# Kernel tuning notes

Hardware: AMD Instinct MI355X
Metric: run time of the kernel (lower is better)

## Reference

```python
import jax, jax.numpy as jnp
import numpy as np

NUM_ENTITIES = 100000
NUM_RELATIONS = 500
D = 256            # embedding_dim
T = 4              # num_hash_tables
H = 32             # hash_dim
B = 64             # batch of queries
K = 10
CAND = max(K * 10, int(NUM_ENTITIES * 0.1))  # = 10000


def setup_inputs() -> dict:
    key = jax.random.key(0)
    k0, k1, k2, k3, k4 = jax.random.split(key, 5)
    return {
        "head": jax.random.randint(k0, (B,), 0, NUM_ENTITIES),
        "relation": jax.random.randint(k1, (B,), 0, NUM_RELATIONS),
        "entity_emb": jax.random.normal(k2, (NUM_ENTITIES, D), jnp.float32) * 0.02,
        "relation_emb": jax.random.normal(k3, (NUM_RELATIONS, D), jnp.float32) * 0.02,
        "hash_proj": jax.random.normal(k4, (T, D, H), jnp.float32),
        "k": K,
    }


def reference(head, relation, entity_emb, relation_emb, hash_proj, k):
    # DistMult approximate query path of KnowledgeGraph.query (use_approximate=True).
    h = entity_emb[head]            # [B, D]
    r = relation_emb[relation]      # [B, D]
    target = h * r                  # DistMult target embedding [B, D]

    # LSH hash codes (0/1 floats): projected > 0
    thash = (jnp.einsum('bd,tdh->bth', target, hash_proj) > 0).astype(jnp.float32)      # [B,T,H]
    ahash = (jnp.einsum('nd,tdh->nth', entity_emb, hash_proj) > 0).astype(jnp.float32)  # [N,T,H]

    # Hamming distance over (T,H) bits without materializing [B,N,T,H]:
    # mismatches = sum(a) + sum(b) - 2 * <a,b>  for 0/1 codes
    dot = jnp.einsum('bth,nth->bn', thash, ahash)                                        # [B,N]
    hash_dist = thash.sum((1, 2))[:, None] + ahash.sum((1, 2))[None, :] - 2.0 * dot      # [B,N]

    # top num_candidates with SMALLEST hamming distance
    _, cand_idx = jax.lax.top_k(-hash_dist, CAND)                                        # [B,CAND]

    # DistMult score: (h*r*t).sum(-1) == target . t ; compute dense then gather candidates
    scores_all = jnp.einsum('bd,nd->bn', target, entity_emb)                             # [B,N]
    cand_scores = jnp.take_along_axis(scores_all, cand_idx, axis=1)                      # [B,CAND]

    top_scores, top_local = jax.lax.top_k(cand_scores, k)                                # [B,k]
    top_indices = jnp.take_along_axis(cand_idx, top_local, axis=1)                       # [B,k]
    return top_indices, top_scores
```

## Files before the change

### kernel.cpp

```cpp
#include <hip/hip_runtime.h>
#include <hip/hip_bf16.h>
#include <float.h>

constexpr int NENT  = 100000;
constexpr int DDIM  = 256;
constexpr int BQ    = 64;
constexpr int CANDN = 10000;
constexpr int KTOP  = 10;
constexpr int NSLICE = 16;
constexpr int SLICE  = 6272;
constexpr int HPAD   = 132;

typedef short v8s __attribute__((ext_vector_type(8)));
typedef float v4f __attribute__((ext_vector_type(4)));

__device__ inline void split3(float x, unsigned short& h0, unsigned short& h1,
                              unsigned short& h2) {
    unsigned t0 = __float_as_uint(x) & 0xffff0000u;
    float r1 = x - __uint_as_float(t0);
    unsigned t1 = __float_as_uint(r1) & 0xffff0000u;
    float r2 = r1 - __uint_as_float(t1);
    h0 = (unsigned short)(t0 >> 16);
    h1 = (unsigned short)(t1 >> 16);
    h2 = (unsigned short)(__float_as_uint(r2) >> 16);
}

__device__ inline void split8(const float* ap, v8s& o0, v8s& o1, v8s& o2) {
    union { v8s v; unsigned short u[8]; } r0, r1, r2;
    float4 f0 = *(const float4*)ap;
    float4 f1 = *(const float4*)(ap + 4);
    float av[8] = {f0.x, f0.y, f0.z, f0.w, f1.x, f1.y, f1.z, f1.w};
    #pragma unroll
    for (int j = 0; j < 8; j++)
        split3(av[j], r0.u[j], r1.u[j], r2.u[j]);
    o0 = r0.v; o1 = r1.v; o2 = r2.v;
}

__global__ __launch_bounds__(128) void k_targets(
    const int* __restrict__ head, const int* __restrict__ rel,
    const float* __restrict__ E, const float* __restrict__ Rm,
    const float* __restrict__ proj,
    float* __restrict__ tgtT, unsigned* __restrict__ thash)
{
    __shared__ float tg[DDIM];
    int b = blockIdx.x;
    int tid = threadIdx.x;
    int h = head[b], r = rel[b];
    for (int d = tid; d < DDIM; d += 128) {
        float v = E[h*DDIM + d] * Rm[r*DDIM + d];
        tg[d] = v;
        tgtT[d*BQ + b] = v;
    }
    __syncthreads();
    int t = tid >> 5, hh = tid & 31;
    float acc = 0.f;
    #pragma unroll 8
    for (int d = 0; d < DDIM; d++)
        acc += tg[d] * proj[(t*DDIM + d)*32 + hh];
    unsigned long long m = __ballot(acc > 0.0f);
    int lane = tid & 63, w = tid >> 6;
    if (lane == 0) {
        thash[b*4 + w*2 + 0] = (unsigned)(m & 0xffffffffull);
        thash[b*4 + w*2 + 1] = (unsigned)(m >> 32);
    }
}

__global__ __launch_bounds__(256) void k_prepw(
    const float* __restrict__ proj, const float* __restrict__ tgtT,
    unsigned short* __restrict__ Whi, unsigned short* __restrict__ Wmid,
    unsigned short* __restrict__ Wlo)
{
    int c = blockIdx.x;
    int d = threadIdx.x;
    float x = (c < 128) ? proj[((c >> 5)*DDIM + d)*32 + (c & 31)]
                        : tgtT[d*BQ + (c - 128)];
    unsigned short h0, h1, h2;
    split3(x, h0, h1, h2);
    Whi [c*DDIM + d] = h0;
    Wmid[c*DDIM + d] = h1;
    Wlo [c*DDIM + d] = h2;
}

constexpr int TILE_E = 128;
constexpr int LSTR = 40;
constexpr int ASTR = 36;

__global__ __launch_bounds__(256, 2) void k_gemm(
    const float* __restrict__ E,
    const unsigned short* __restrict__ Whi, const unsigned short* __restrict__ Wmid,
    const unsigned short* __restrict__ Wlo,
    unsigned* __restrict__ ahash, float* __restrict__ scores)
{
    __shared__ __align__(16) float Af[TILE_E*ASTR];
    __shared__ __align__(16) unsigned short Bhi[192*LSTR];
    __shared__ __align__(16) unsigned short Bmid[192*LSTR];
    __shared__ __align__(16) unsigned short Blo[192*LSTR];
    unsigned short* bitsHalf = (unsigned short*)Af;

    int tid = threadIdx.x;
    int l = tid & 63, w = tid >> 6;
    int wm = w >> 1, wn = w & 1;
    int m = l & 15, quad = l >> 4;
    int n0 = blockIdx.x * TILE_E;

    v4f acc[4][6];
    #pragma unroll
    for (int a = 0; a < 4; a++)
        #pragma unroll
        for (int c = 0; c < 6; c++)
            acc[a][c] = (v4f)0.0f;

    for (int ch = 0; ch < DDIM/32; ch++) {
        int d0 = ch * 32;
        __syncthreads();
        #pragma unroll
        for (int it = 0; it < 4; it++) {
            int idx = tid + it*256;
            int row = idx >> 3;
            int kq  = (idx & 7) * 4;
            int n = n0 + row; if (n >= NENT) n = NENT - 1;
            *(float4*)&Af[row*ASTR + kq] = *(const float4*)(E + (size_t)n*DDIM + d0 + kq);
        }
        #pragma unroll
        for (int it = 0; it < 3; it++) {
            int idx = tid + it*256;
            int col = idx >> 2;
            int k8  = (idx & 3) * 8;
            *(uint4*)&Bhi [col*LSTR + k8] = *(const uint4*)(Whi  + col*DDIM + d0 + k8);
            *(uint4*)&Bmid[col*LSTR + k8] = *(const uint4*)(Wmid + col*DDIM + d0 + k8);
            *(uint4*)&Blo [col*LSTR + k8] = *(const uint4*)(Wlo  + col*DDIM + d0 + k8);
        }
        __syncthreads();
        v8s a0[4], a1[4], a2[4];
        #pragma unroll
        for (int a = 0; a < 4; a++)
            split8(&Af[(wm*64 + a*16 + m)*ASTR + quad*8], a0[a], a1[a], a2[a]);
        #pragma unroll
        for (int c = 0; c < 6; c++) {
            int co = (wn*96 + c*16 + m)*LSTR + quad*8;
            v8s b0 = *(const v8s*)&Bhi [co];
            v8s b1 = *(const v8s*)&Bmid[co];
            v8s b2 = *(const v8s*)&Blo [co];
            #pragma unroll
            for (int a = 0; a < 4; a++) {
                acc[a][c] = __builtin_amdgcn_mfma_f32_16x16x32_bf16(a2[a], b0, acc[a][c], 0, 0, 0);
                acc[a][c] = __builtin_amdgcn_mfma_f32_16x16x32_bf16(a0[a], b2, acc[a][c], 0, 0, 0);
                acc[a][c] = __builtin_amdgcn_mfma_f32_16x16x32_bf16(a1[a], b1, acc[a][c], 0, 0, 0);
                acc[a][c] = __builtin_amdgcn_mfma_f32_16x16x32_bf16(a1[a], b0, acc[a][c], 0, 0, 0);
                acc[a][c] = __builtin_amdgcn_mfma_f32_16x16x32_bf16(a0[a], b1, acc[a][c], 0, 0, 0);
                acc[a][c] = __builtin_amdgcn_mfma_f32_16x16x32_bf16(a0[a], b0, acc[a][c], 0, 0, 0);
            }
        }
    }

    __syncthreads();
    #pragma unroll
    for (int c = 0; c < 6; c++) {
        int ct = wn*6 + c;
        if (ct < 8) {
            #pragma unroll
            for (int a = 0; a < 4; a++) {
                #pragma unroll
                for (int r = 0; r < 4; r++) {
                    unsigned long long mb = __ballot(acc[a][c][r] > 0.0f);
                    if (m == 0) {
                        int rowl = wm*64 + a*16 + quad*4 + r;
                        bitsHalf[rowl*8 + ct] = (unsigned short)(mb >> (quad*16));
                    }
                }
            }
        } else {
            int b = ct*16 - 128 + m;
            #pragma unroll
            for (int a = 0; a < 4; a++) {
                int nb = n0 + wm*64 + a*16 + quad*4;
                if (nb < NENT)
                    *(float4*)(scores + (size_t)b*NENT + nb) = *(float4*)&acc[a][c];
            }
        }
    }
    __syncthreads();
    if (tid < TILE_E) {
        int n = n0 + tid;
        if (n < NENT)
            *(uint4*)(ahash + (size_t)n*4) = *(const uint4*)&bitsHalf[tid*8];
    }
}

__global__ __launch_bounds__(256) void k_dist(
    const unsigned* __restrict__ ahash, const unsigned* __restrict__ thash,
    unsigned char* __restrict__ dist8, unsigned short* __restrict__ histG)
{
    __shared__ unsigned hist[HPAD];
    int s = blockIdx.x, b = blockIdx.y, tid = threadIdx.x;
    for (int i = tid; i < HPAD; i += 256) hist[i] = 0u;
    uint4 tw = *(const uint4*)(thash + b*4);
    __syncthreads();
    int n0 = s*SLICE;
    int n1 = n0 + SLICE; if (n1 > NENT) n1 = NENT;
    unsigned char* drow = dist8 + (size_t)b*NENT;
    for (int n = n0 + tid*4; n < n1; n += 1024) {
        int dv[4];
        #pragma unroll
        for (int i = 0; i < 4; i++) {
            uint4 a = *(const uint4*)(ahash + (size_t)(n+i)*4);
            dv[i] = __popc(a.x^tw.x) + __popc(a.y^tw.y) +
                    __popc(a.z^tw.z) + __popc(a.w^tw.w);
            atomicAdd(&hist[dv[i]], 1u);
        }
        uchar4 o = make_uchar4((unsigned char)dv[0], (unsigned char)dv[1],
                               (unsigned char)dv[2], (unsigned char)dv[3]);
        *(uchar4*)(drow + n) = o;
    }
    __syncthreads();
    unsigned short* hrow = histG + ((size_t)b*NSLICE + s)*HPAD;
    for (int i = tid; i < 129; i += 256) hrow[i] = (unsigned short)hist[i];
}

__global__ __launch_bounds__(64) void k_cut(
    const unsigned char* __restrict__ dist8, const unsigned short* __restrict__ histG,
    int* __restrict__ dsG, int* __restrict__ ncG)
{
    __shared__ unsigned histT[HPAD];
    __shared__ int dsS, slS, rpS;
    int b = blockIdx.x, tid = threadIdx.x;
    for (int d = tid; d < 129; d += 64) {
        unsigned sum = 0;
        for (int s = 0; s < NSLICE; s++)
            sum += histG[((size_t)b*NSLICE + s)*HPAD + d];
        histT[d] = sum;
    }
    __syncthreads();
    if (tid == 0) {
        unsigned cum = 0; int ds = 128; unsigned R = 1;
        for (int d = 0; d < 129; d++) {
            unsigned c = cum + histT[d];
            if (c >= (unsigned)CANDN) { ds = d; R = (unsigned)CANDN - cum; break; }
            cum = c;
        }
        dsS = ds; dsG[b] = ds;
        unsigned acc = 0;
        for (int s = 0; s < NSLICE; s++) {
            unsigned c = histG[((size_t)b*NSLICE + s)*HPAD + ds];
            if (acc + c >= R) { slS = s; rpS = (int)(R - acc); break; }
            acc += c;
        }
    }
    __syncthreads();
    int ds = dsS;
    unsigned Rp = (unsigned)rpS;
    const unsigned char* drow = dist8 + (size_t)b*NENT;
    int sBase = slS*SLICE;
    int sEnd = sBase + SLICE; if (sEnd > NENT) sEnd = NENT;
    unsigned cnt = 0;
    for (int base = sBase; base < sEnd; base += 64) {
        int n = base + tid;
        bool eq = (n < sEnd) && (drow[n] == (unsigned char)ds);
        unsigned long long mm = __ballot(eq);
        unsigned c = __popcll(mm);
        if (cnt + c >= Rp) {
            unsigned pre = __popcll(mm & ((1ull << tid) - 1ull));
            if (eq && (cnt + pre + 1u == Rp)) ncG[b] = n;
            break;
        }
        cnt += c;
    }
}

__global__ __launch_bounds__(256) void k_part(
    const unsigned char* __restrict__ dist8, const float* __restrict__ scores,
    const int* __restrict__ dsG, const int* __restrict__ ncG,
    const float* __restrict__ tgtT, const float* __restrict__ E,
    float* __restrict__ partS, int* __restrict__ partI)
{
    __shared__ float rs[256];
    __shared__ int   ri[256];
    __shared__ int   rt[256];
    __shared__ int   chosenI[KTOP];
    __shared__ float tgl[DDIM];

    int sl = blockIdx.x, b = blockIdx.y, tid = threadIdx.x;
    int ds = dsG[b], nc = ncG[b];
    const unsigned char* drow = dist8 + (size_t)b*NENT;
    const float* srow = scores + (size_t)b*NENT;
    int n0 = sl*SLICE;
    int n1 = n0 + SLICE; if (n1 > NENT) n1 = NENT;

    float topS[KTOP]; int topI[KTOP];
    #pragma unroll
    for (int i = 0; i < KTOP; i++) { topS[i] = -FLT_MAX; topI[i] = 0x7fffffff; }

    for (int n = n0 + tid*4; n < n1; n += 1024) {
        uchar4 dv = *(const uchar4*)(drow + n);
        unsigned char da[4] = {dv.x, dv.y, dv.z, dv.w};
        #pragma unroll
        for (int i = 0; i < 4; i++) {
            int d = da[i];
            int nn = n + i;
            if (d < ds || (d == ds && nn <= nc)) {
                float sc = srow[nn];
                if (sc > topS[KTOP-1]) {
                    int p = KTOP - 1;
                    while (p > 0 && topS[p-1] < sc) {
                        topS[p] = topS[p-1]; topI[p] = topI[p-1]; p--;
                    }
                    topS[p] = sc; topI[p] = nn;
                }
            }
        }
    }

    int ph = 0;
    for (int r = 0; r < KTOP; r++) {
        rs[tid] = topS[ph]; ri[tid] = topI[ph]; rt[tid] = tid;
        __syncthreads();
        for (int st = 128; st > 0; st >>= 1) {
            if (tid < st) {
                bool take = (rs[tid+st] > rs[tid]) ||
                            (rs[tid+st] == rs[tid] && ri[tid+st] < ri[tid]);
                if (take) { rs[tid]=rs[tid+st]; ri[tid]=ri[tid+st]; rt[tid]=rt[tid+st]; }
            }
            __syncthreads();
        }
        if (tid == 0) {
            chosenI[r] = ri[0];
            partI[((size_t)b*NSLICE + sl)*KTOP + r] = ri[0];
        }
        int winner = rt[0];
        __syncthreads();
        if (tid == winner) ph++;
        __syncthreads();
    }

    for (int d = tid; d < DDIM; d += 256) tgl[d] = tgtT[d*BQ + b];
    __syncthreads();
    if (tid < KTOP) {
        int idx = chosenI[tid];
        float sc = -FLT_MAX;
        if (idx >= 0 && idx < NENT) {
            const float* er = E + (size_t)idx*DDIM;
            float acc = 0.f;
            #pragma unroll 8
            for (int d = 0; d < DDIM; d += 4) {
                float4 v = *(const float4*)(er + d);
                acc += v.x*tgl[d+0];
                acc += v.y*tgl[d+1];
                acc += v.z*tgl[d+2];
                acc += v.w*tgl[d+3];
            }
            sc = acc;
        }
        partS[((size_t)b*NSLICE + sl)*KTOP + tid] = sc;
    }
}

__global__ __launch_bounds__(256) void k_merge(
    const float* __restrict__ partS, const int* __restrict__ partI,
    float* __restrict__ out)
{
    __shared__ float sc2[NSLICE*KTOP];
    __shared__ int   ix2[NSLICE*KTOP];
    int b = blockIdx.x, tid = threadIdx.x;
    if (tid < NSLICE*KTOP) {
        sc2[tid] = partS[(size_t)b*NSLICE*KTOP + tid];
        ix2[tid] = partI[(size_t)b*NSLICE*KTOP + tid];
    }
    __syncthreads();
    if (tid < NSLICE*KTOP) {
        float mv = sc2[tid]; int mi = ix2[tid];
        int rank = 0;
        #pragma unroll 8
        for (int i = 0; i < NSLICE*KTOP; i++) {
            float v = sc2[i]; int id = ix2[i];
            bool beats = (v > mv) ||
                         (v == mv && (id < mi || (id == mi && i < tid)));
            rank += beats ? 1 : 0;
        }
        if (rank < KTOP) {
            out[b*KTOP + rank]           = (float)mi;
            out[BQ*KTOP + b*KTOP + rank] = mv;
        }
    }
}

extern "C" void kernel_launch(void* const* d_in, const int* in_sizes, int n_in,
                              void* d_out, int out_size, void* d_ws, size_t ws_size,
                              hipStream_t stream)
{
    const int*   head = (const int*)d_in[0];
    const int*   rel  = (const int*)d_in[1];
    const float* E    = (const float*)d_in[2];
    const float* Rm   = (const float*)d_in[3];
    const float* proj = (const float*)d_in[4];

    char* ws = (char*)d_ws;
    float*          tgtT   = (float*)(ws);
    unsigned*       thash  = (unsigned*)(ws + 65536);
    unsigned*       ahash  = (unsigned*)(ws + 66560);
    float*          scores = (float*)(ws + 1666560);
    unsigned char*  dist8  = (unsigned char*)(ws + 27266560);
    int*            dsG    = (int*)(ws + 33666560);
    int*            ncG    = (int*)(ws + 33666816);
    float*          partS  = (float*)(ws + 33667072);
    int*            partI  = (int*)(ws + 33708032);
    unsigned short* histG  = (unsigned short*)(ws + 33748992);
    unsigned short* Whi    = (unsigned short*)(ws + 34019328);
    unsigned short* Wmid   = (unsigned short*)(ws + 34117632);
    unsigned short* Wlo    = (unsigned short*)(ws + 34215936);
    float*          out    = (float*)d_out;

    hipLaunchKernelGGL(k_targets, dim3(BQ), dim3(128), 0, stream,
                       head, rel, E, Rm, proj, tgtT, thash);
    hipLaunchKernelGGL(k_prepw, dim3(192), dim3(256), 0, stream,
                       proj, tgtT, Whi, Wmid, Wlo);
    hipLaunchKernelGGL(k_gemm, dim3((NENT + TILE_E - 1)/TILE_E), dim3(256), 0, stream,
                       E, Whi, Wmid, Wlo, ahash, scores);
    hipLaunchKernelGGL(k_dist, dim3(NSLICE, BQ), dim3(256), 0, stream,
                       ahash, thash, dist8, histG);
    hipLaunchKernelGGL(k_cut, dim3(BQ), dim3(64), 0, stream,
                       dist8, histG, dsG, ncG);
    hipLaunchKernelGGL(k_part, dim3(NSLICE, BQ), dim3(256), 0, stream,
                       dist8, scores, dsG, ncG, tgtT, E, partS, partI);
    hipLaunchKernelGGL(k_merge, dim3(BQ), dim3(256), 0, stream,
                       partS, partI, out);
}
```

Measured before the change: 358.1 us.

## Double-buffer entity tiles via direct global-to-LDS loads and per-wave histograms

The GEMM kernel now stages the entity tile into a double-buffered, XOR-swizzled LDS area using global_load_lds, so the next chunk is prefetched while the current one is split and fed to MFMA. It also drops the LDS staging of the bf16 weight splits and reads them straight from global memory. Separately, the distance kernel keeps one histogram per wave to cut LDS atomic contention, then sums them at the end. The changes trade LDS footprint and sync structure for overlap. They risk extra global read traffic for the weights and a possible race, because no explicit wait guards the async LDS load before its buffer is used.

```diff
diff --git a/kernel.cpp b/kernel.cpp
--- a/kernel.cpp
+++ b/kernel.cpp
@@ -25,15 +25,22 @@
     h2 = (unsigned short)(__float_as_uint(r2) >> 16);
 }
 
-__device__ inline void split8(const float* ap, v8s& o0, v8s& o1, v8s& o2) {
+__device__ inline void split8p(const float* p0, const float* p1,
+                               v8s& o0, v8s& o1, v8s& o2) {
     union { v8s v; unsigned short u[8]; } r0, r1, r2;
-    float4 f0 = *(const float4*)ap;
-    float4 f1 = *(const float4*)(ap + 4);
+    float4 f0 = *(const float4*)p0;
+    float4 f1 = *(const float4*)(p1);
     float av[8] = {f0.x, f0.y, f0.z, f0.w, f1.x, f1.y, f1.z, f1.w};
     #pragma unroll
     for (int j = 0; j < 8; j++)
         split3(av[j], r0.u[j], r1.u[j], r2.u[j]);
     o0 = r0.v; o1 = r1.v; o2 = r2.v;
+}
+
+__device__ inline void stage16(const float* g, float* l) {
+    __builtin_amdgcn_global_load_lds(
+        (const __attribute__((address_space(1))) void*)g,
+        (__attribute__((address_space(3))) void*)l, 16, 0, 0);
 }
 
 __global__ __launch_bounds__(128) void k_targets(
@@ -82,8 +89,6 @@
 }
 
 constexpr int TILE_E = 128;
-constexpr int LSTR = 40;
-constexpr int ASTR = 36;
 
 __global__ __launch_bounds__(256, 2) void k_gemm(
     const float* __restrict__ E,
@@ -91,10 +96,7 @@
     const unsigned short* __restrict__ Wlo,
     unsigned* __restrict__ ahash, float* __restrict__ scores)
 {
-    __shared__ __align__(16) float Af[TILE_E*ASTR];
-    __shared__ __align__(16) unsigned short Bhi[192*LSTR];
-    __shared__ __align__(16) unsigned short Bmid[192*LSTR];
-    __shared__ __align__(16) unsigned short Blo[192*LSTR];
+    __shared__ __align__(16) float Af[2][TILE_E*32];
     unsigned short* bitsHalf = (unsigned short*)Af;
 
     int tid = threadIdx.x;
@@ -103,6 +105,29 @@
     int m = l & 15, quad = l >> 4;
     int n0 = blockIdx.x * TILE_E;
 
+    const float* gsrc[4];
+    #pragma unroll
+    for (int it = 0; it < 4; it++) {
+        int U = it*256 + tid;
+        int row = U >> 3;
+        int us  = (U & 7) ^ (row & 7);
+        int n = n0 + row; if (n >= NENT) n = NENT - 1;
+        gsrc[it] = E + (size_t)n*DDIM + us*4;
+    }
+
+    int offA0[4], offA1[4];
+    #pragma unroll
+    for (int a = 0; a < 4; a++) {
+        int row = wm*64 + a*16 + m;
+        offA0[a] = row*32 + (((2*quad)    ) ^ (m & 7))*4;
+        offA1[a] = row*32 + (((2*quad) | 1) ^ (m & 7))*4;
+    }
+
+    int colOff[6];
+    #pragma unroll
+    for (int c = 0; c < 6; c++)
+        colOff[c] = (wn*96 + c*16 + m)*DDIM + quad*8;
+
     v4f acc[4][6];
     #pragma unroll
     for (int a = 0; a < 4; a++)
@@ -110,37 +135,32 @@
         for (int c = 0; c < 6; c++)
             acc[a][c] = (v4f)0.0f;
 
+    #pragma unroll
+    for (int it = 0; it < 4; it++)
+        stage16(gsrc[it], &Af[0][(it*256 + w*64)*4]);
+    __syncthreads();
+
+    int bb = 0;
     for (int ch = 0; ch < DDIM/32; ch++) {
-        int d0 = ch * 32;
-        __syncthreads();
-        #pragma unroll
-        for (int it = 0; it < 4; it++) {
-            int idx = tid + it*256;
-            int row = idx >> 3;
-            int kq  = (idx & 7) * 4;
-            int n = n0 + row; if (n >= NENT) n = NENT - 1;
-            *(float4*)&Af[row*ASTR + kq] = *(const float4*)(E + (size_t)n*DDIM + d0 + kq);
-        }
-        #pragma unroll
-        for (int it = 0; it < 3; it++) {
-            int idx = tid + it*256;
-            int col = idx >> 2;
-            int k8  = (idx & 3) * 8;
-            *(uint4*)&Bhi [col*LSTR + k8] = *(const uint4*)(Whi  + col*DDIM + d0 + k8);
-            *(uint4*)&Bmid[col*LSTR + k8] = *(const uint4*)(Wmid + col*DDIM + d0 + k8);
-            *(uint4*)&Blo [col*LSTR + k8] = *(const uint4*)(Wlo  + col*DDIM + d0 + k8);
-        }
-        __syncthreads();
+        if (ch + 1 < DDIM/32) {
+            const float* gadd = (const float*)((const char*)0) ; (void)gadd;
+            #pragma unroll
+            for (int it = 0; it < 4; it++)
+                stage16(gsrc[it] + (ch + 1)*32, &Af[bb ^ 1][(it*256 + w*64)*4]);
+        }
+
         v8s a0[4], a1[4], a2[4];
         #pragma unroll
         for (int a = 0; a < 4; a++)
-            split8(&Af[(wm*64 + a*16 + m)*ASTR + quad*8], a0[a], a1[a], a2[a]);
+            split8p(&Af[bb][offA0[a]], &Af[bb][offA1[a]], a0[a], a1[a], a2[a]);
+
+        int d0 = ch*32;
         #pragma unroll
         for (int c = 0; c < 6; c++) {
-            int co = (wn*96 + c*16 + m)*LSTR + quad*8;
-            v8s b0 = *(const v8s*)&Bhi [co];
-            v8s b1 = *(const v8s*)&Bmid[co];
-            v8s b2 = *(const v8s*)&Blo [co];
+            int co = colOff[c] + d0;
+            v8s b0 = *(const v8s*)(Whi  + co);
+            v8s b1 = *(const v8s*)(Wmid + co);
+            v8s b2 = *(const v8s*)(Wlo  + co);
             #pragma unroll
             for (int a = 0; a < 4; a++) {
                 acc[a][c] = __builtin_amdgcn_mfma_f32_16x16x32_bf16(a2[a], b0, acc[a][c], 0, 0, 0);
@@ -151,9 +171,10 @@
                 acc[a][c] = __builtin_amdgcn_mfma_f32_16x16x32_bf16(a0[a], b0, acc[a][c], 0, 0, 0);
             }
         }
-    }
-
-    __syncthreads();
+        __syncthreads();
+        bb ^= 1;
+    }
+
     #pragma unroll
     for (int c = 0; c < 6; c++) {
         int ct = wn*6 + c;
@@ -191,9 +212,10 @@
     const unsigned* __restrict__ ahash, const unsigned* __restrict__ thash,
     unsigned char* __restrict__ dist8, unsigned short* __restrict__ histG)
 {
-    __shared__ unsigned hist[HPAD];
+    __shared__ unsigned hist[4][HPAD];
     int s = blockIdx.x, b = blockIdx.y, tid = threadIdx.x;
-    for (int i = tid; i < HPAD; i += 256) hist[i] = 0u;
+    int wv = tid >> 6;
+    for (int i = tid; i < 4*HPAD; i += 256) ((unsigned*)hist)[i] = 0u;
     uint4 tw = *(const uint4*)(thash + b*4);
     __syncthreads();
     int n0 = s*SLICE;
@@ -206,7 +228,7 @@
             uint4 a = *(const uint4*)(ahash + (size_t)(n+i)*4);
             dv[i] = __popc(a.x^tw.x) + __popc(a.y^tw.y) +
                     __popc(a.z^tw.z) + __popc(a.w^tw.w);
-            atomicAdd(&hist[dv[i]], 1u);
+            atomicAdd(&hist[wv][dv[i]], 1u);
         }
         uchar4 o = make_uchar4((unsigned char)dv[0], (unsigned char)dv[1],
                                (unsigned char)dv[2], (unsigned char)dv[3]);
@@ -214,7 +236,8 @@
     }
     __syncthreads();
     unsigned short* hrow = histG + ((size_t)b*NSLICE + s)*HPAD;
-    for (int i = tid; i < 129; i += 256) hrow[i] = (unsigned short)hist[i];
+    for (int i = tid; i < 129; i += 256)
+        hrow[i] = (unsigned short)(hist[0][i] + hist[1][i] + hist[2][i] + hist[3][i]);
 }
 
 __global__ __launch_bounds__(64) void k_cut(
```

Result: faster. 347.5 us (-3.0%).
